# Kernel tuning notes

Measured on AMD Instinct MI355X. Metric: run time of the kernel, lower is better.

Reference implementation:

```python
import jax, jax.numpy as jnp
import numpy as np

D_MODEL = 512
SEQ_LEN = 2048
S = 32  # local window size
BATCH = 2


def setup_inputs() -> dict:
    key = jax.random.key(0)
    ks = jax.random.split(key, 12)
    shp = (SEQ_LEN, BATCH, D_MODEL)
    return {
        "query": jax.random.normal(ks[0], shp, jnp.float32),
        "key": jax.random.normal(ks[1], shp, jnp.float32),
        "value": jax.random.normal(ks[2], shp, jnp.float32),
        "Wq": jax.random.normal(ks[3], (D_MODEL, D_MODEL), jnp.float32) * 0.02,
        "bq": jax.random.normal(ks[4], (D_MODEL,), jnp.float32) * 0.01,
        "Wk": jax.random.normal(ks[5], (D_MODEL, D_MODEL), jnp.float32) * 0.02,
        "bk": jax.random.normal(ks[6], (D_MODEL,), jnp.float32) * 0.01,
        "Wv": jax.random.normal(ks[7], (D_MODEL, D_MODEL), jnp.float32) * 0.02,
        "bv": jax.random.normal(ks[8], (D_MODEL,), jnp.float32) * 0.01,
        "pos_bias": jax.random.normal(ks[9], (SEQ_LEN, SEQ_LEN), jnp.float32) * 0.02,
        "Wo": jax.random.normal(ks[10], (D_MODEL, D_MODEL), jnp.float32) * 0.02,
        "bo": jax.random.normal(ks[11], (D_MODEL,), jnp.float32) * 0.01,
    }


def _aft_local(query, key, value, Wq, bq, Wk, bk, Wv, bv, pos_bias, Wo, bo):
    T, B, D = query.shape
    q = query @ Wq.T + bq  # [T,B,D]
    k = key @ Wk.T + bk
    v = value @ Wv.T + bv
    pb = pos_bias[:T, :T]

    # max_logit: elementwise max of per-dim key max and (key + col-max of pos_bias) max,
    # then batch index 0 (faithful to original `[0]` indexing) -> shape [D]
    max_logit = jnp.maximum(k.max(axis=0),
                            (k + pb.max(axis=0)[:, None, None]).max(axis=0))[0]

    # out-of-window running sums: tokens t' <= t - S contribute exp(k) (no pos bias)
    ek = jnp.exp(k - max_logit)                 # [T,B,D]
    cs_num = jnp.cumsum(ek * v, axis=0)
    cs_den = jnp.cumsum(ek, axis=0)
    t_arr = jnp.arange(T)
    prefix_idx = jnp.clip(t_arr - S, 0, T - 1)
    has_prefix = (t_arr >= S)[:, None, None]
    num_out = jnp.where(has_prefix, cs_num[prefix_idx], 0.0)
    den_out = jnp.where(has_prefix, cs_den[prefix_idx], 0.0)

    # in-window part: t' in [max(0, t-S+1), t] with pos_bias[t, t']
    j = jnp.arange(S)
    idx_raw = t_arr[:, None] - S + 1 + j[None, :]   # [T,S]
    valid = (idx_raw >= 0).astype(k.dtype)
    idx = jnp.clip(idx_raw, 0, T - 1)
    k_win = k[idx]                                  # [T,S,B,D]
    v_win = v[idx]                                  # [T,S,B,D]
    pb_win = pb[t_arr[:, None], idx]                # [T,S]
    exp_l = jnp.exp(k_win + pb_win[:, :, None, None] - max_logit) * valid[:, :, None, None]
    num_in = (exp_l * v_win).sum(axis=1)            # [T,B,D]
    den_in = exp_l.sum(axis=1)

    y = jax.nn.sigmoid(q) * (num_out + num_in) / (den_out + den_in)
    return y @ Wo.T + bo


def reference(query, key, value, Wq, bq, Wk, bk, Wv, bv, pos_bias, Wo, bo):
    return _aft_local(query, key, value, Wq, bq, Wk, bk, Wv, bv, pos_bias, Wo, bo)
```

## Files before the change

### kernel.cpp

```cpp
#include <hip/hip_runtime.h>
#include <hip/hip_bf16.h>

#define TT 2048
#define BB 2
#define DD 512
#define BD (BB*DD)
#define SS 32
#define MR (TT*BB)
#define NE (TT*BB*DD)
#define CH 32

typedef __bf16 bf16x8 __attribute__((ext_vector_type(8)));
typedef float f32x4 __attribute__((ext_vector_type(4)));
typedef float f32x2 __attribute__((ext_vector_type(2)));

__device__ __forceinline__ void async_copy16(void* lds, const void* gptr) {
    __builtin_amdgcn_global_load_lds(
        (const __attribute__((address_space(1))) void*)gptr,
        (__attribute__((address_space(3))) void*)lds,
        16, 0, 0);
}

#define MFMA16(a,b,c) __builtin_amdgcn_mfma_f32_16x16x32_bf16((a),(b),(c),0,0,0)

__global__ __launch_bounds__(256) void cast_all(
    const float* __restrict__ s0, const float* __restrict__ s1, const float* __restrict__ s2,
    const float* __restrict__ w0, const float* __restrict__ w1,
    const float* __restrict__ w2, const float* __restrict__ w3,
    __hip_bfloat16* __restrict__ d0, __hip_bfloat16* __restrict__ d1, __hip_bfloat16* __restrict__ d2,
    __hip_bfloat16* __restrict__ e0, __hip_bfloat16* __restrict__ e1,
    __hip_bfloat16* __restrict__ e2, __hip_bfloat16* __restrict__ e3)
{
    int b = blockIdx.x;
    const float* s;
    __hip_bfloat16* d;
    size_t i;
    if (b < 6144) {
        int which = b >> 11;
        s = which == 0 ? s0 : (which == 1 ? s1 : s2);
        d = which == 0 ? d0 : (which == 1 ? d1 : d2);
        i = ((size_t)(b & 2047) * 256 + threadIdx.x) * 4;
    } else {
        int b2 = b - 6144;
        int which = b2 >> 8;
        s = which == 0 ? w0 : (which == 1 ? w1 : (which == 2 ? w2 : w3));
        d = which == 0 ? e0 : (which == 1 ? e1 : (which == 2 ? e2 : e3));
        i = ((size_t)(b2 & 255) * 256 + threadIdx.x) * 4;
    }
    float4 f = *(const float4*)(s + i);
    union { __hip_bfloat16 h[4]; ushort4 u; } cv;
    cv.h[0] = __float2bfloat16(f.x); cv.h[1] = __float2bfloat16(f.y);
    cv.h[2] = __float2bfloat16(f.z); cv.h[3] = __float2bfloat16(f.w);
    *(ushort4*)((unsigned short*)d + i) = cv.u;
}

__global__ __launch_bounds__(256) void gemm_qkv(
    const __hip_bfloat16* __restrict__ qb, const __hip_bfloat16* __restrict__ kb,
    const __hip_bfloat16* __restrict__ vb,
    const __hip_bfloat16* __restrict__ Wqb, const __hip_bfloat16* __restrict__ Wkb,
    const __hip_bfloat16* __restrict__ Wvb,
    const float* __restrict__ bq, const float* __restrict__ bk,
    const float* __restrict__ bv,
    float* __restrict__ qout, float* __restrict__ ekn,
    float* __restrict__ part)
{
    __shared__ char smem[49152];
    const int tid = threadIdx.x;
    const int lane = tid & 63;
    const int wv = tid >> 6;
    const int wave_m = wv >> 1, wave_n = wv & 1;
    const int flat = blockIdx.x + 8 * blockIdx.y;
    const int mt = flat & 63, nt = flat >> 6;
    const int m0 = mt * 64, n0 = nt * 64;
    const int kq = lane >> 4, rr = lane & 15;

    if (blockIdx.z == 0) {
        f32x4 acc[2][2] = {};
        const __hip_bfloat16* Arow = qb + (size_t)(m0 + lane) * DD + wv * 8;
        const __hip_bfloat16* Wrow = Wqb + (size_t)(n0 + lane) * DD + wv * 8;
        async_copy16(smem + 0*8192 +        wv*1024, Arow + 0);
        async_copy16(smem + 0*8192 + 4096 + wv*1024, Wrow + 0);
        async_copy16(smem + 1*8192 +        wv*1024, Arow + 32);
        async_copy16(smem + 1*8192 + 4096 + wv*1024, Wrow + 32);
        asm volatile("s_waitcnt vmcnt(2)" ::: "memory");
        __builtin_amdgcn_s_barrier();
        #pragma unroll
        for (int it = 0; it < 16; ++it) {
            if (it + 2 < 16) {
                char* nb = smem + ((it + 2) % 3) * 8192;
                async_copy16(nb +        wv*1024, Arow + (it+2)*32);
                async_copy16(nb + 4096 + wv*1024, Wrow + (it+2)*32);
            }
            const char* cb = smem + (it % 3) * 8192;
            bf16x8 a0 = *(const bf16x8*)(cb + kq*1024 + (wave_m*32 +  0 + rr)*16);
            bf16x8 a1 = *(const bf16x8*)(cb + kq*1024 + (wave_m*32 + 16 + rr)*16);
            bf16x8 w0 = *(const bf16x8*)(cb + 4096 + kq*1024 + (wave_n*32 +  0 + rr)*16);
            bf16x8 w1 = *(const bf16x8*)(cb + 4096 + kq*1024 + (wave_n*32 + 16 + rr)*16);
            acc[0][0] = MFMA16(a0, w0, acc[0][0]);
            acc[0][1] = MFMA16(a0, w1, acc[0][1]);
            acc[1][0] = MFMA16(a1, w0, acc[1][0]);
            acc[1][1] = MFMA16(a1, w1, acc[1][1]);
            if (it < 15) {
                if (it < 14) asm volatile("s_waitcnt vmcnt(2) lgkmcnt(0)" ::: "memory");
                else         asm volatile("s_waitcnt vmcnt(0) lgkmcnt(0)" ::: "memory");
                __builtin_amdgcn_s_barrier();
            }
        }
        #pragma unroll
        for (int ms = 0; ms < 2; ++ms)
            #pragma unroll
            for (int ns = 0; ns < 2; ++ns) {
                int n = n0 + wave_n*32 + ns*16 + rr;
                float bn = bq[n];
                #pragma unroll
                for (int r = 0; r < 4; ++r) {
                    int m = m0 + wave_m*32 + ms*16 + kq*4 + r;
                    float x = acc[ms][ns][r] + bn;
                    qout[(size_t)m * DD + n] = 1.f / (1.f + expf(-x));
                }
            }
    } else {
        f32x4 acck[2][2] = {}, accv[2][2] = {};
        const __hip_bfloat16* AKrow = kb + (size_t)(m0 + lane) * DD + wv * 8;
        const __hip_bfloat16* WKrow = Wkb + (size_t)(n0 + lane) * DD + wv * 8;
        const __hip_bfloat16* AVrow = vb + (size_t)(m0 + lane) * DD + wv * 8;
        const __hip_bfloat16* WVrow = Wvb + (size_t)(n0 + lane) * DD + wv * 8;
        #pragma unroll
        for (int pt = 0; pt < 2; ++pt) {
            char* nb = smem + pt * 16384;
            async_copy16(nb +         wv*1024, AKrow + pt*32);
            async_copy16(nb +  4096 + wv*1024, WKrow + pt*32);
            async_copy16(nb +  8192 + wv*1024, AVrow + pt*32);
            async_copy16(nb + 12288 + wv*1024, WVrow + pt*32);
        }
        asm volatile("s_waitcnt vmcnt(4)" ::: "memory");
        __builtin_amdgcn_s_barrier();
        #pragma unroll
        for (int it = 0; it < 16; ++it) {
            if (it + 2 < 16) {
                char* nb = smem + ((it + 2) % 3) * 16384;
                async_copy16(nb +         wv*1024, AKrow + (it+2)*32);
                async_copy16(nb +  4096 + wv*1024, WKrow + (it+2)*32);
                async_copy16(nb +  8192 + wv*1024, AVrow + (it+2)*32);
                async_copy16(nb + 12288 + wv*1024, WVrow + (it+2)*32);
            }
            const char* cb = smem + (it % 3) * 16384;
            bf16x8 ak0 = *(const bf16x8*)(cb +         kq*1024 + (wave_m*32 +  0 + rr)*16);
            bf16x8 ak1 = *(const bf16x8*)(cb +         kq*1024 + (wave_m*32 + 16 + rr)*16);
            bf16x8 bk0 = *(const bf16x8*)(cb +  4096 + kq*1024 + (wave_n*32 +  0 + rr)*16);
            bf16x8 bk1 = *(const bf16x8*)(cb +  4096 + kq*1024 + (wave_n*32 + 16 + rr)*16);
            bf16x8 av0 = *(const bf16x8*)(cb +  8192 + kq*1024 + (wave_m*32 +  0 + rr)*16);
            bf16x8 av1 = *(const bf16x8*)(cb +  8192 + kq*1024 + (wave_m*32 + 16 + rr)*16);
            bf16x8 bv0 = *(const bf16x8*)(cb + 12288 + kq*1024 + (wave_n*32 +  0 + rr)*16);
            bf16x8 bv1 = *(const bf16x8*)(cb + 12288 + kq*1024 + (wave_n*32 + 16 + rr)*16);
            acck[0][0] = MFMA16(ak0, bk0, acck[0][0]);
            acck[0][1] = MFMA16(ak0, bk1, acck[0][1]);
            acck[1][0] = MFMA16(ak1, bk0, acck[1][0]);
            acck[1][1] = MFMA16(ak1, bk1, acck[1][1]);
            accv[0][0] = MFMA16(av0, bv0, accv[0][0]);
            accv[0][1] = MFMA16(av0, bv1, accv[0][1]);
            accv[1][0] = MFMA16(av1, bv0, accv[1][0]);
            accv[1][1] = MFMA16(av1, bv1, accv[1][1]);
            if (it < 15) {
                if (it < 14) asm volatile("s_waitcnt vmcnt(4) lgkmcnt(0)" ::: "memory");
                else         asm volatile("s_waitcnt vmcnt(0) lgkmcnt(0)" ::: "memory");
                __builtin_amdgcn_s_barrier();
            }
        }
        float sd[2][2] = {{0.f,0.f},{0.f,0.f}};
        float sn[2][2] = {{0.f,0.f},{0.f,0.f}};
        #pragma unroll
        for (int ms = 0; ms < 2; ++ms)
            #pragma unroll
            for (int ns = 0; ns < 2; ++ns) {
                int n = n0 + wave_n*32 + ns*16 + rr;
                float bkn = bk[n], bvn = bv[n];
                #pragma unroll
                for (int r = 0; r < 4; ++r) {
                    int m = m0 + wave_m*32 + ms*16 + kq*4 + r;
                    float e  = expf(acck[ms][ns][r] + bkn);
                    float nv = e * (accv[ms][ns][r] + bvn);
                    float2 st; st.x = e; st.y = nv;
                    *(float2*)&ekn[((size_t)m * DD + n) * 2] = st;
                    sd[ns][r & 1] += e;
                    sn[ns][r & 1] += nv;
                }
            }
        #pragma unroll
        for (int ns = 0; ns < 2; ++ns)
            #pragma unroll
            for (int par = 0; par < 2; ++par) {
                sd[ns][par] += __shfl_xor(sd[ns][par], 16, 64);
                sd[ns][par] += __shfl_xor(sd[ns][par], 32, 64);
                sn[ns][par] += __shfl_xor(sn[ns][par], 16, 64);
                sn[ns][par] += __shfl_xor(sn[ns][par], 32, 64);
            }
        __syncthreads();
        float* red = (float*)smem;
        if (lane < 16) {
            #pragma unroll
            for (int ns = 0; ns < 2; ++ns) {
                int c2 = wave_n*32 + ns*16 + rr;
                red[(0*2 + wave_m)*64 + c2] = sd[ns][0];
                red[(1*2 + wave_m)*64 + c2] = sd[ns][1];
                red[(2*2 + wave_m)*64 + c2] = sn[ns][0];
                red[(3*2 + wave_m)*64 + c2] = sn[ns][1];
            }
        }
        __syncthreads();
        {
            int which = tid >> 6;
            int c2 = tid & 63;
            float s = red[(which*2 + 0)*64 + c2] + red[(which*2 + 1)*64 + c2];
            int b = which & 1;
            int sel = which >> 1;
            part[((size_t)mt * BD + b*512 + n0 + c2) * 2 + sel] = s;
        }
    }
}

__global__ __launch_bounds__(256, 3) void fused_window(
    const float* __restrict__ qf, const float* __restrict__ ekn,
    const float* __restrict__ part, const float* __restrict__ pb,
    __hip_bfloat16* __restrict__ yb)
{
    __shared__ float Et[64 * 64 * 2];
    __shared__ float wl[CH][SS];
    __shared__ float red[4 * 64 * 2];
    const int tid = threadIdx.x;
    const int chunk = blockIdx.y;
    const int t0 = chunk * CH;
    const int col0 = blockIdx.x * 64;
    const int c = tid & 63;
    const int sg = tid >> 6;
    const int s0 = sg * 8;

    {
        const int cp = tid & 31;
        #pragma unroll
        for (int j = 0; j < 8; ++j) {
            int u = (tid >> 5) + j * 8;
            int t = t0 - 32 + u;
            if (t >= 0) {
                const void* g = (const void*)(ekn + ((size_t)t * BD + col0 + cp * 2) * 2);
                async_copy16((char*)Et + (tid >> 6) * 1024 + j * 4096, g);
            }
        }
        if (chunk == 0) {
            f32x4 z = {0.f, 0.f, 0.f, 0.f};
            #pragma unroll
            for (int j = 0; j < 4; ++j)
                *(f32x4*)((char*)Et + tid * 16 + j * 4096) = z;
        }
    }

    #pragma unroll
    for (int i = 0; i < (CH * SS) / 256; ++i) {
        int idx = tid + i * 256;
        int tl = idx >> 5, jj = idx & 31;
        int t = t0 + tl;
        int u2 = t - (SS - 1) + jj;
        float w = 0.f;
        if (u2 >= 0) w = expf(pb[(size_t)t * TT + u2]);
        wl[tl][jj] = w;
    }

    float qv[8];
    #pragma unroll
    for (int k = 0; k < 8; ++k)
        qv[k] = qf[(size_t)(t0 + s0 + k) * BD + col0 + c];
    f32x2 acc2 = {0.f, 0.f};
    #pragma unroll
    for (int j = 0; j < 16; ++j) {
        int p = sg + 4 * j;
        if (p < chunk)
            acc2 += *(const f32x2*)&part[((size_t)p * BD + col0 + c) * 2];
    }
    *(f32x2*)&red[(sg * 64 + c) * 2] = acc2;

    __syncthreads();

    f32x2 P = *(const f32x2*)&red[(0 * 64 + c) * 2];
    P += *(const f32x2*)&red[(1 * 64 + c) * 2];
    P += *(const f32x2*)&red[(2 * 64 + c) * 2];
    P += *(const f32x2*)&red[(3 * 64 + c) * 2];

    f32x2 ring[39];
    #pragma unroll
    for (int i = 0; i < 39; ++i)
        ring[i] = *(const f32x2*)&Et[((s0 + 1 + i) * 64 + c) * 2];

    f32x2 cs = P;
    if (sg == 0) {
        #pragma unroll
        for (int i = 0; i < 31; ++i) cs -= ring[i];
    } else if (sg == 1) {
        #pragma unroll
        for (int i = 0; i < 23; ++i) cs -= ring[i];
    } else if (sg == 2) {
        #pragma unroll
        for (int i = 0; i < 15; ++i) cs -= ring[i];
    } else {
        #pragma unroll
        for (int i = 0; i < 7; ++i) cs -= ring[i];
    }

    #pragma unroll
    for (int k = 0; k < 8; ++k) {
        int s = s0 + k;
        if (k > 0) cs += ring[k - 1];
        f32x2 acc = cs;
        #pragma unroll
        for (int j4 = 0; j4 < 8; ++j4) {
            float4 w4 = *(const float4*)&wl[s][j4 * 4];
            acc += w4.x * ring[k + j4*4 + 0];
            acc += w4.y * ring[k + j4*4 + 1];
            acc += w4.z * ring[k + j4*4 + 2];
            acc += w4.w * ring[k + j4*4 + 3];
        }
        yb[(size_t)(t0 + s) * BD + col0 + c] = __float2bfloat16(qv[k] * acc.y / acc.x);
    }
}

__global__ __launch_bounds__(256) void gemm_out(
    const __hip_bfloat16* __restrict__ yb, const __hip_bfloat16* __restrict__ Wob,
    const float* __restrict__ bo, float* __restrict__ out)
{
    __shared__ char smem[24576];
    const int tid = threadIdx.x;
    const int lane = tid & 63;
    const int wv = tid >> 6;
    const int wave_m = wv >> 1, wave_n = wv & 1;
    const int flat = blockIdx.x + 8 * blockIdx.y;
    const int mt = flat & 63, nt = flat >> 6;
    const int m0 = mt * 64, n0 = nt * 64;
    const int kq = lane >> 4, rr = lane & 15;

    f32x4 acc[2][2] = {};
    const __hip_bfloat16* Arow = yb + (size_t)(m0 + lane) * DD + wv * 8;
    const __hip_bfloat16* Wrow = Wob + (size_t)(n0 + lane) * DD + wv * 8;

    async_copy16(smem + 0*8192 +        wv*1024, Arow + 0);
    async_copy16(smem + 0*8192 + 4096 + wv*1024, Wrow + 0);
    async_copy16(smem + 1*8192 +        wv*1024, Arow + 32);
    async_copy16(smem + 1*8192 + 4096 + wv*1024, Wrow + 32);
    asm volatile("s_waitcnt vmcnt(2)" ::: "memory");
    __builtin_amdgcn_s_barrier();
    #pragma unroll
    for (int it = 0; it < 16; ++it) {
        if (it + 2 < 16) {
            char* nb = smem + ((it + 2) % 3) * 8192;
            async_copy16(nb +        wv*1024, Arow + (it+2)*32);
            async_copy16(nb + 4096 + wv*1024, Wrow + (it+2)*32);
        }
        const char* cb = smem + (it % 3) * 8192;
        bf16x8 a0 = *(const bf16x8*)(cb + kq*1024 + (wave_m*32 +  0 + rr)*16);
        bf16x8 a1 = *(const bf16x8*)(cb + kq*1024 + (wave_m*32 + 16 + rr)*16);
        bf16x8 w0 = *(const bf16x8*)(cb + 4096 + kq*1024 + (wave_n*32 +  0 + rr)*16);
        bf16x8 w1 = *(const bf16x8*)(cb + 4096 + kq*1024 + (wave_n*32 + 16 + rr)*16);
        acc[0][0] = MFMA16(a0, w0, acc[0][0]);
        acc[0][1] = MFMA16(a0, w1, acc[0][1]);
        acc[1][0] = MFMA16(a1, w0, acc[1][0]);
        acc[1][1] = MFMA16(a1, w1, acc[1][1]);
        if (it < 15) {
            if (it < 14) asm volatile("s_waitcnt vmcnt(2) lgkmcnt(0)" ::: "memory");
            else         asm volatile("s_waitcnt vmcnt(0) lgkmcnt(0)" ::: "memory");
            __builtin_amdgcn_s_barrier();
        }
    }
    #pragma unroll
    for (int ms = 0; ms < 2; ++ms)
        #pragma unroll
        for (int ns = 0; ns < 2; ++ns) {
            int n = n0 + wave_n*32 + ns*16 + rr;
            float bn = bo[n];
            #pragma unroll
            for (int r = 0; r < 4; ++r) {
                int m = m0 + wave_m*32 + ms*16 + kq*4 + r;
                out[(size_t)m * DD + n] = acc[ms][ns][r] + bn;
            }
        }
}

extern "C" void kernel_launch(void* const* d_in, const int* in_sizes, int n_in,
                              void* d_out, int out_size, void* d_ws, size_t ws_size,
                              hipStream_t stream) {
    const float* query = (const float*)d_in[0];
    const float* key   = (const float*)d_in[1];
    const float* value = (const float*)d_in[2];
    const float* Wq    = (const float*)d_in[3];
    const float* bq    = (const float*)d_in[4];
    const float* Wk    = (const float*)d_in[5];
    const float* bk    = (const float*)d_in[6];
    const float* Wv    = (const float*)d_in[7];
    const float* bv    = (const float*)d_in[8];
    const float* pb    = (const float*)d_in[9];
    const float* Wo    = (const float*)d_in[10];
    const float* bo    = (const float*)d_in[11];
    float* out = (float*)d_out;

    float* ws = (float*)d_ws;
    float* qf   = ws;
    float* ekn  = ws + (size_t)NE;
    float* part = ws + (size_t)3 * NE;
    __hip_bfloat16* bfb = (__hip_bfloat16*)(part + 131072);
    __hip_bfloat16* qb  = bfb;
    __hip_bfloat16* kb  = bfb + (size_t)NE;
    __hip_bfloat16* vb  = bfb + (size_t)2 * NE;
    __hip_bfloat16* yb  = bfb + (size_t)3 * NE;
    __hip_bfloat16* Wqb = bfb + (size_t)4 * NE;
    __hip_bfloat16* Wkb = Wqb + 262144;
    __hip_bfloat16* Wvb = Wkb + 262144;
    __hip_bfloat16* Wob = Wvb + 262144;

    cast_all<<<7168, 256, 0, stream>>>(query, key, value, Wq, Wk, Wv, Wo,
                                       qb, kb, vb, Wqb, Wkb, Wvb, Wob);

    gemm_qkv<<<dim3(DD / 64, MR / 64, 2), 256, 0, stream>>>(
        qb, kb, vb, Wqb, Wkb, Wvb, bq, bk, bv,
        qf, ekn, part);

    fused_window<<<dim3(BD / 64, TT / CH), 256, 0, stream>>>(
        qf, ekn, part, pb, yb);

    gemm_out<<<dim3(DD / 64, MR / 64), 256, 0, stream>>>(yb, Wob, bo, out);
}
```

Baseline: 153.6 us.

## Fuse fp32-to-bf16 cast into GEMM tile loads and drop cast kernel

Removes the separate cast_all kernel. The QKV and output GEMMs now stream fp32 inputs and weights straight into LDS and convert them to bf16 at fragment-load time. This saves a kernel launch and the round trip of writing and re-reading the bf16 copies. In exchange each GEMM moves twice the bytes per tile and does conversions in its inner loop. The K/V path also drops from a triple-buffer prefetch depth of two to double buffering with a full vmcnt(0) wait each iteration, which may expose load latency.

```diff
diff --git a/kernel.cpp b/kernel.cpp
--- a/kernel.cpp
+++ b/kernel.cpp
@@ -23,48 +23,28 @@
 
 #define MFMA16(a,b,c) __builtin_amdgcn_mfma_f32_16x16x32_bf16((a),(b),(c),0,0,0)
 
-__global__ __launch_bounds__(256) void cast_all(
-    const float* __restrict__ s0, const float* __restrict__ s1, const float* __restrict__ s2,
-    const float* __restrict__ w0, const float* __restrict__ w1,
-    const float* __restrict__ w2, const float* __restrict__ w3,
-    __hip_bfloat16* __restrict__ d0, __hip_bfloat16* __restrict__ d1, __hip_bfloat16* __restrict__ d2,
-    __hip_bfloat16* __restrict__ e0, __hip_bfloat16* __restrict__ e1,
-    __hip_bfloat16* __restrict__ e2, __hip_bfloat16* __restrict__ e3)
-{
-    int b = blockIdx.x;
-    const float* s;
-    __hip_bfloat16* d;
-    size_t i;
-    if (b < 6144) {
-        int which = b >> 11;
-        s = which == 0 ? s0 : (which == 1 ? s1 : s2);
-        d = which == 0 ? d0 : (which == 1 ? d1 : d2);
-        i = ((size_t)(b & 2047) * 256 + threadIdx.x) * 4;
-    } else {
-        int b2 = b - 6144;
-        int which = b2 >> 8;
-        s = which == 0 ? w0 : (which == 1 ? w1 : (which == 2 ? w2 : w3));
-        d = which == 0 ? e0 : (which == 1 ? e1 : (which == 2 ? e2 : e3));
-        i = ((size_t)(b2 & 255) * 256 + threadIdx.x) * 4;
-    }
-    float4 f = *(const float4*)(s + i);
-    union { __hip_bfloat16 h[4]; ushort4 u; } cv;
-    cv.h[0] = __float2bfloat16(f.x); cv.h[1] = __float2bfloat16(f.y);
-    cv.h[2] = __float2bfloat16(f.z); cv.h[3] = __float2bfloat16(f.w);
-    *(ushort4*)((unsigned short*)d + i) = cv.u;
+__device__ __forceinline__ bf16x8 ldcvt(const char* p) {
+    f32x4 x = *(const f32x4*)p;
+    f32x4 y = *(const f32x4*)(p + 16);
+    union { __hip_bfloat16 h[8]; bf16x8 v; } u;
+    u.h[0] = __float2bfloat16(x[0]); u.h[1] = __float2bfloat16(x[1]);
+    u.h[2] = __float2bfloat16(x[2]); u.h[3] = __float2bfloat16(x[3]);
+    u.h[4] = __float2bfloat16(y[0]); u.h[5] = __float2bfloat16(y[1]);
+    u.h[6] = __float2bfloat16(y[2]); u.h[7] = __float2bfloat16(y[3]);
+    return u.v;
 }
 
 __global__ __launch_bounds__(256) void gemm_qkv(
-    const __hip_bfloat16* __restrict__ qb, const __hip_bfloat16* __restrict__ kb,
-    const __hip_bfloat16* __restrict__ vb,
-    const __hip_bfloat16* __restrict__ Wqb, const __hip_bfloat16* __restrict__ Wkb,
-    const __hip_bfloat16* __restrict__ Wvb,
+    const float* __restrict__ query, const float* __restrict__ key,
+    const float* __restrict__ value,
+    const float* __restrict__ Wq, const float* __restrict__ Wk,
+    const float* __restrict__ Wv,
     const float* __restrict__ bq, const float* __restrict__ bk,
     const float* __restrict__ bv,
     float* __restrict__ qout, float* __restrict__ ekn,
     float* __restrict__ part)
 {
-    __shared__ char smem[49152];
+    __shared__ char smem[65536];
     const int tid = threadIdx.x;
     const int lane = tid & 63;
     const int wv = tid >> 6;
@@ -73,39 +53,43 @@
     const int mt = flat & 63, nt = flat >> 6;
     const int m0 = mt * 64, n0 = nt * 64;
     const int kq = lane >> 4, rr = lane & 15;
+    const int srow  = ((wv & 1) << 5) + (lane >> 1);
+    const int skq0  = (wv >> 1);
+    const int shalf = (lane & 1) * 4;
 
     if (blockIdx.z == 0) {
         f32x4 acc[2][2] = {};
-        const __hip_bfloat16* Arow = qb + (size_t)(m0 + lane) * DD + wv * 8;
-        const __hip_bfloat16* Wrow = Wqb + (size_t)(n0 + lane) * DD + wv * 8;
-        async_copy16(smem + 0*8192 +        wv*1024, Arow + 0);
-        async_copy16(smem + 0*8192 + 4096 + wv*1024, Wrow + 0);
-        async_copy16(smem + 1*8192 +        wv*1024, Arow + 32);
-        async_copy16(smem + 1*8192 + 4096 + wv*1024, Wrow + 32);
-        asm volatile("s_waitcnt vmcnt(2)" ::: "memory");
+        const float* a0s = query + (size_t)(m0 + srow) * DD + skq0 * 8 + shalf;
+        const float* a1s = a0s + 16;
+        const float* w0s = Wq    + (size_t)(n0 + srow) * DD + skq0 * 8 + shalf;
+        const float* w1s = w0s + 16;
+#define STQ(b, t) { \
+        async_copy16(smem + (b)*16384 +        0 + wv*1024, a0s + (t)*32); \
+        async_copy16(smem + (b)*16384 +     4096 + wv*1024, a1s + (t)*32); \
+        async_copy16(smem + (b)*16384 + 8192 + 0 + wv*1024, w0s + (t)*32); \
+        async_copy16(smem + (b)*16384 + 8192+4096 + wv*1024, w1s + (t)*32); }
+        STQ(0, 0); STQ(1, 1);
+        asm volatile("s_waitcnt vmcnt(4)" ::: "memory");
         __builtin_amdgcn_s_barrier();
         #pragma unroll
         for (int it = 0; it < 16; ++it) {
-            if (it + 2 < 16) {
-                char* nb = smem + ((it + 2) % 3) * 8192;
-                async_copy16(nb +        wv*1024, Arow + (it+2)*32);
-                async_copy16(nb + 4096 + wv*1024, Wrow + (it+2)*32);
-            }
-            const char* cb = smem + (it % 3) * 8192;
-            bf16x8 a0 = *(const bf16x8*)(cb + kq*1024 + (wave_m*32 +  0 + rr)*16);
-            bf16x8 a1 = *(const bf16x8*)(cb + kq*1024 + (wave_m*32 + 16 + rr)*16);
-            bf16x8 w0 = *(const bf16x8*)(cb + 4096 + kq*1024 + (wave_n*32 +  0 + rr)*16);
-            bf16x8 w1 = *(const bf16x8*)(cb + 4096 + kq*1024 + (wave_n*32 + 16 + rr)*16);
+            if (it + 2 < 16) STQ((it + 2) % 3, it + 2);
+            const char* cb = smem + (it % 3) * 16384;
+            bf16x8 a0 = ldcvt(cb +        kq*2048 + (wave_m*32 +  0 + rr)*32);
+            bf16x8 a1 = ldcvt(cb +        kq*2048 + (wave_m*32 + 16 + rr)*32);
+            bf16x8 w0 = ldcvt(cb + 8192 + kq*2048 + (wave_n*32 +  0 + rr)*32);
+            bf16x8 w1 = ldcvt(cb + 8192 + kq*2048 + (wave_n*32 + 16 + rr)*32);
             acc[0][0] = MFMA16(a0, w0, acc[0][0]);
             acc[0][1] = MFMA16(a0, w1, acc[0][1]);
             acc[1][0] = MFMA16(a1, w0, acc[1][0]);
             acc[1][1] = MFMA16(a1, w1, acc[1][1]);
             if (it < 15) {
-                if (it < 14) asm volatile("s_waitcnt vmcnt(2) lgkmcnt(0)" ::: "memory");
+                if (it < 14) asm volatile("s_waitcnt vmcnt(4) lgkmcnt(0)" ::: "memory");
                 else         asm volatile("s_waitcnt vmcnt(0) lgkmcnt(0)" ::: "memory");
                 __builtin_amdgcn_s_barrier();
             }
         }
+#undef STQ
         #pragma unroll
         for (int ms = 0; ms < 2; ++ms)
             #pragma unroll
@@ -121,38 +105,38 @@
             }
     } else {
         f32x4 acck[2][2] = {}, accv[2][2] = {};
-        const __hip_bfloat16* AKrow = kb + (size_t)(m0 + lane) * DD + wv * 8;
-        const __hip_bfloat16* WKrow = Wkb + (size_t)(n0 + lane) * DD + wv * 8;
-        const __hip_bfloat16* AVrow = vb + (size_t)(m0 + lane) * DD + wv * 8;
-        const __hip_bfloat16* WVrow = Wvb + (size_t)(n0 + lane) * DD + wv * 8;
-        #pragma unroll
-        for (int pt = 0; pt < 2; ++pt) {
-            char* nb = smem + pt * 16384;
-            async_copy16(nb +         wv*1024, AKrow + pt*32);
-            async_copy16(nb +  4096 + wv*1024, WKrow + pt*32);
-            async_copy16(nb +  8192 + wv*1024, AVrow + pt*32);
-            async_copy16(nb + 12288 + wv*1024, WVrow + pt*32);
-        }
-        asm volatile("s_waitcnt vmcnt(4)" ::: "memory");
+        const float* ak0s = key   + (size_t)(m0 + srow) * DD + skq0 * 8 + shalf;
+        const float* ak1s = ak0s + 16;
+        const float* wk0s = Wk    + (size_t)(n0 + srow) * DD + skq0 * 8 + shalf;
+        const float* wk1s = wk0s + 16;
+        const float* av0s = value + (size_t)(m0 + srow) * DD + skq0 * 8 + shalf;
+        const float* av1s = av0s + 16;
+        const float* wv0s = Wv    + (size_t)(n0 + srow) * DD + skq0 * 8 + shalf;
+        const float* wv1s = wv0s + 16;
+#define ST1(b, t) { \
+        async_copy16(smem + (b)*32768 +         0 + wv*1024, ak0s + (t)*32); \
+        async_copy16(smem + (b)*32768 +      4096 + wv*1024, ak1s + (t)*32); \
+        async_copy16(smem + (b)*32768 +  8192 + 0 + wv*1024, wk0s + (t)*32); \
+        async_copy16(smem + (b)*32768 +  8192+4096 + wv*1024, wk1s + (t)*32); \
+        async_copy16(smem + (b)*32768 + 16384 + 0 + wv*1024, av0s + (t)*32); \
+        async_copy16(smem + (b)*32768 + 16384+4096 + wv*1024, av1s + (t)*32); \
+        async_copy16(smem + (b)*32768 + 24576 + 0 + wv*1024, wv0s + (t)*32); \
+        async_copy16(smem + (b)*32768 + 24576+4096 + wv*1024, wv1s + (t)*32); }
+        ST1(0, 0);
+        asm volatile("s_waitcnt vmcnt(0)" ::: "memory");
         __builtin_amdgcn_s_barrier();
         #pragma unroll
         for (int it = 0; it < 16; ++it) {
-            if (it + 2 < 16) {
-                char* nb = smem + ((it + 2) % 3) * 16384;
-                async_copy16(nb +         wv*1024, AKrow + (it+2)*32);
-                async_copy16(nb +  4096 + wv*1024, WKrow + (it+2)*32);
-                async_copy16(nb +  8192 + wv*1024, AVrow + (it+2)*32);
-                async_copy16(nb + 12288 + wv*1024, WVrow + (it+2)*32);
-            }
-            const char* cb = smem + (it % 3) * 16384;
-            bf16x8 ak0 = *(const bf16x8*)(cb +         kq*1024 + (wave_m*32 +  0 + rr)*16);
-            bf16x8 ak1 = *(const bf16x8*)(cb +         kq*1024 + (wave_m*32 + 16 + rr)*16);
-            bf16x8 bk0 = *(const bf16x8*)(cb +  4096 + kq*1024 + (wave_n*32 +  0 + rr)*16);
-            bf16x8 bk1 = *(const bf16x8*)(cb +  4096 + kq*1024 + (wave_n*32 + 16 + rr)*16);
-            bf16x8 av0 = *(const bf16x8*)(cb +  8192 + kq*1024 + (wave_m*32 +  0 + rr)*16);
-            bf16x8 av1 = *(const bf16x8*)(cb +  8192 + kq*1024 + (wave_m*32 + 16 + rr)*16);
-            bf16x8 bv0 = *(const bf16x8*)(cb + 12288 + kq*1024 + (wave_n*32 +  0 + rr)*16);
-            bf16x8 bv1 = *(const bf16x8*)(cb + 12288 + kq*1024 + (wave_n*32 + 16 + rr)*16);
+            if (it + 1 < 16) ST1((it + 1) & 1, it + 1);
+            const char* cb = smem + (it & 1) * 32768;
+            bf16x8 ak0 = ldcvt(cb +         kq*2048 + (wave_m*32 +  0 + rr)*32);
+            bf16x8 ak1 = ldcvt(cb +         kq*2048 + (wave_m*32 + 16 + rr)*32);
+            bf16x8 bk0 = ldcvt(cb +  8192 + kq*2048 + (wave_n*32 +  0 + rr)*32);
+            bf16x8 bk1 = ldcvt(cb +  8192 + kq*2048 + (wave_n*32 + 16 + rr)*32);
+            bf16x8 av0 = ldcvt(cb + 16384 + kq*2048 + (wave_m*32 +  0 + rr)*32);
+            bf16x8 av1 = ldcvt(cb + 16384 + kq*2048 + (wave_m*32 + 16 + rr)*32);
+            bf16x8 bv0 = ldcvt(cb + 24576 + kq*2048 + (wave_n*32 +  0 + rr)*32);
+            bf16x8 bv1 = ldcvt(cb + 24576 + kq*2048 + (wave_n*32 + 16 + rr)*32);
             acck[0][0] = MFMA16(ak0, bk0, acck[0][0]);
             acck[0][1] = MFMA16(ak0, bk1, acck[0][1]);
             acck[1][0] = MFMA16(ak1, bk0, acck[1][0]);
@@ -162,11 +146,11 @@
             accv[1][0] = MFMA16(av1, bv0, accv[1][0]);
             accv[1][1] = MFMA16(av1, bv1, accv[1][1]);
             if (it < 15) {
-                if (it < 14) asm volatile("s_waitcnt vmcnt(4) lgkmcnt(0)" ::: "memory");
-                else         asm volatile("s_waitcnt vmcnt(0) lgkmcnt(0)" ::: "memory");
+                asm volatile("s_waitcnt vmcnt(0) lgkmcnt(0)" ::: "memory");
                 __builtin_amdgcn_s_barrier();
             }
         }
+#undef ST1
         float sd[2][2] = {{0.f,0.f},{0.f,0.f}};
         float sn[2][2] = {{0.f,0.f},{0.f,0.f}};
         #pragma unroll
@@ -323,10 +307,10 @@
 }
 
 __global__ __launch_bounds__(256) void gemm_out(
-    const __hip_bfloat16* __restrict__ yb, const __hip_bfloat16* __restrict__ Wob,
+    const __hip_bfloat16* __restrict__ yb, const float* __restrict__ Wo,
     const float* __restrict__ bo, float* __restrict__ out)
 {
-    __shared__ char smem[24576];
+    __shared__ char smem[36864];
     const int tid = threadIdx.x;
     const int lane = tid & 63;
     const int wv = tid >> 6;
@@ -335,39 +319,40 @@
     const int mt = flat & 63, nt = flat >> 6;
     const int m0 = mt * 64, n0 = nt * 64;
     const int kq = lane >> 4, rr = lane & 15;
+    const int srow  = ((wv & 1) << 5) + (lane >> 1);
+    const int skq0  = (wv >> 1);
+    const int shalf = (lane & 1) * 4;
 
     f32x4 acc[2][2] = {};
     const __hip_bfloat16* Arow = yb + (size_t)(m0 + lane) * DD + wv * 8;
-    const __hip_bfloat16* Wrow = Wob + (size_t)(n0 + lane) * DD + wv * 8;
-
-    async_copy16(smem + 0*8192 +        wv*1024, Arow + 0);
-    async_copy16(smem + 0*8192 + 4096 + wv*1024, Wrow + 0);
-    async_copy16(smem + 1*8192 +        wv*1024, Arow + 32);
-    async_copy16(smem + 1*8192 + 4096 + wv*1024, Wrow + 32);
-    asm volatile("s_waitcnt vmcnt(2)" ::: "memory");
+    const float* w0s = Wo + (size_t)(n0 + srow) * DD + skq0 * 8 + shalf;
+    const float* w1s = w0s + 16;
+#define STO(b, t) { \
+    async_copy16(smem + (b)*12288 +           wv*1024, Arow + (t)*32); \
+    async_copy16(smem + (b)*12288 + 4096 +    wv*1024, w0s + (t)*32); \
+    async_copy16(smem + (b)*12288 + 4096+4096 + wv*1024, w1s + (t)*32); }
+    STO(0, 0); STO(1, 1);
+    asm volatile("s_waitcnt vmcnt(3)" ::: "memory");
     __builtin_amdgcn_s_barrier();
     #pragma unroll
     for (int it = 0; it < 16; ++it) {
-        if (it + 2 < 16) {
-            char* nb = smem + ((it + 2) % 3) * 8192;
-            async_copy16(nb +        wv*1024, Arow + (it+2)*32);
-            async_copy16(nb + 4096 + wv*1024, Wrow + (it+2)*32);
-        }
-        const char* cb = smem + (it % 3) * 8192;
+        if (it + 2 < 16) STO((it + 2) % 3, it + 2);
+        const char* cb = smem + (it % 3) * 12288;
         bf16x8 a0 = *(const bf16x8*)(cb + kq*1024 + (wave_m*32 +  0 + rr)*16);
         bf16x8 a1 = *(const bf16x8*)(cb + kq*1024 + (wave_m*32 + 16 + rr)*16);
-        bf16x8 w0 = *(const bf16x8*)(cb + 4096 + kq*1024 + (wave_n*32 +  0 + rr)*16);
-        bf16x8 w1 = *(const bf16x8*)(cb + 4096 + kq*1024 + (wave_n*32 + 16 + rr)*16);
+        bf16x8 w0 = ldcvt(cb + 4096 + kq*2048 + (wave_n*32 +  0 + rr)*32);
+        bf16x8 w1 = ldcvt(cb + 4096 + kq*2048 + (wave_n*32 + 16 + rr)*32);
         acc[0][0] = MFMA16(a0, w0, acc[0][0]);
         acc[0][1] = MFMA16(a0, w1, acc[0][1]);
         acc[1][0] = MFMA16(a1, w0, acc[1][0]);
         acc[1][1] = MFMA16(a1, w1, acc[1][1]);
         if (it < 15) {
-            if (it < 14) asm volatile("s_waitcnt vmcnt(2) lgkmcnt(0)" ::: "memory");
+            if (it < 14) asm volatile("s_waitcnt vmcnt(3) lgkmcnt(0)" ::: "memory");
             else         asm volatile("s_waitcnt vmcnt(0) lgkmcnt(0)" ::: "memory");
             __builtin_amdgcn_s_barrier();
         }
     }
+#undef STO
     #pragma unroll
     for (int ms = 0; ms < 2; ++ms)
         #pragma unroll
@@ -403,25 +388,14 @@
     float* qf   = ws;
     float* ekn  = ws + (size_t)NE;
     float* part = ws + (size_t)3 * NE;
-    __hip_bfloat16* bfb = (__hip_bfloat16*)(part + 131072);
-    __hip_bfloat16* qb  = bfb;
-    __hip_bfloat16* kb  = bfb + (size_t)NE;
-    __hip_bfloat16* vb  = bfb + (size_t)2 * NE;
-    __hip_bfloat16* yb  = bfb + (size_t)3 * NE;
-    __hip_bfloat16* Wqb = bfb + (size_t)4 * NE;
-    __hip_bfloat16* Wkb = Wqb + 262144;
-    __hip_bfloat16* Wvb = Wkb + 262144;
-    __hip_bfloat16* Wob = Wvb + 262144;
-
-    cast_all<<<7168, 256, 0, stream>>>(query, key, value, Wq, Wk, Wv, Wo,
-                                       qb, kb, vb, Wqb, Wkb, Wvb, Wob);
+    __hip_bfloat16* yb = (__hip_bfloat16*)(part + 131072);
 
     gemm_qkv<<<dim3(DD / 64, MR / 64, 2), 256, 0, stream>>>(
-        qb, kb, vb, Wqb, Wkb, Wvb, bq, bk, bv,
+        query, key, value, Wq, Wk, Wv, bq, bk, bv,
         qf, ekn, part);
 
     fused_window<<<dim3(BD / 64, TT / CH), 256, 0, stream>>>(
         qf, ekn, part, pb, yb);
 
-    gemm_out<<<dim3(DD / 64, MR / 64), 256, 0, stream>>>(yb, Wob, bo, out);
-}
+    gemm_out<<<dim3(DD / 64, MR / 64), 256, 0, stream>>>(yb, Wo, bo, out);
+}
```

Measured after the change: 155.5 us. Within noise of the previous version (+1.3%).
